# Optimization experiments

Hardware: AMD Instinct MI355X
Metric: run time of the kernel (lower is better)

The kernel has to match this reference:

```python
import jax, jax.numpy as jnp
import numpy as np

N_NODES = 50000
N_EDGES = 800000
N_IN = 256
N_H = 64


def _xavier(key, fan_in, fan_out):
    limit = np.sqrt(6.0 / (fan_in + fan_out)).astype(np.float32)
    return jax.random.uniform(key, (fan_in, fan_out), jnp.float32, -limit, limit)


def setup_inputs() -> dict:
    key = jax.random.key(0)
    ks = jax.random.split(key, 12)
    inp = {
        "bf": jax.random.normal(ks[0], (1, N_NODES, N_IN), jnp.float32),
        "bl": jax.random.normal(ks[1], (1, N_NODES, N_IN), jnp.float32),
        "shuf_fts": jax.random.normal(ks[2], (1, N_NODES, N_IN), jnp.float32),
        "shuf_fls": jax.random.normal(ks[3], (1, N_NODES, N_IN), jnp.float32),
        "adj_rows": jax.random.randint(ks[4], (N_EDGES,), 0, N_NODES, jnp.int32),
        "adj_cols": jax.random.randint(ks[5], (N_EDGES,), 0, N_NODES, jnp.int32),
        "adj_w": jax.random.uniform(ks[6], (N_EDGES,), jnp.float32),
        "diff_rows": jax.random.randint(ks[7], (N_EDGES,), 0, N_NODES, jnp.int32),
        "diff_cols": jax.random.randint(ks[8], (N_EDGES,), 0, N_NODES, jnp.int32),
        "diff_w": jax.random.uniform(ks[9], (N_EDGES,), jnp.float32),
        # GCN parameters (Linear has bias=False; separate additive bias init 0; PReLU slope 0.25)
        "W1": _xavier(ks[10], N_IN, N_H),
        "b1": jnp.zeros((N_H,), jnp.float32),
        "a1": jnp.float32(0.25),
        "W2": _xavier(ks[11], N_IN, N_H),
        "b2": jnp.zeros((N_H,), jnp.float32),
        "a2": jnp.float32(0.25),
    }
    return inp


def _gcn(seq, W, b, a, rows, cols, w):
    # seq: [1, N, F_in]; sparse spmm: out[r] = sum_e 1[rows[e]==r] * w[e] * fts[cols[e]]
    fts = seq[0] @ W                                   # [N, n_h]
    msgs = w[:, None] * fts[cols]                      # [E, n_h] gather
    agg = jax.ops.segment_sum(msgs, rows, num_segments=N_NODES)  # [N, n_h] scatter-add
    out = agg[None, :, :] + b                          # bias add
    return jnp.where(out >= 0, out, a * out)           # PReLU


def reference(bf, bl, shuf_fts, shuf_fls, adj_rows, adj_cols, adj_w,
              diff_rows, diff_cols, diff_w, W1, b1, a1, W2, b2, a2):
    h_1 = _gcn(bf, W1, b1, a1, adj_rows, adj_cols, adj_w)
    h_2 = _gcn(bl, W2, b2, a2, diff_rows, diff_cols, diff_w)
    h_3 = _gcn(shuf_fts, W1, b1, a1, adj_rows, adj_cols, adj_w)
    h_4 = _gcn(shuf_fls, W2, b2, a2, diff_rows, diff_cols, diff_w)
    return jnp.stack([h_1, h_2, h_3, h_4])             # [4, 1, N, n_h]
```

## Files before the change

kernel.cpp:

```cpp
#include <hip/hip_runtime.h>
#include <hip/hip_bf16.h>

#define N_NODES 50000
#define N_EDGES 800000
#define N_IN    256
#define N_H     64
#define NB      125
#define RPB     400
#define BCAP    8192
#define EPT     8
#define BIN_BLK 2048
#define GSTRIDE 264

typedef short short8 __attribute__((ext_vector_type(8)));
typedef float f32x4  __attribute__((ext_vector_type(4)));

__device__ inline short f2bf(float f) {
    __bf16 h = (__bf16)f;
    return (short)__builtin_bit_cast(unsigned short, h);
}
__device__ inline float bflo(unsigned int q) { return __uint_as_float(q << 16); }
__device__ inline float bfhi(unsigned int q) { return __uint_as_float(q & 0xFFFF0000u); }


__global__ __launch_bounds__(256) void k_bin(
    const int* __restrict__ adj_rows, const int* __restrict__ adj_cols,
    const float* __restrict__ adj_w,
    const int* __restrict__ diff_rows, const int* __restrict__ diff_cols,
    const float* __restrict__ diff_w,
    int* __restrict__ gcnt, int2* __restrict__ bin) {

    int g = blockIdx.y;
    const int*   rows = g ? diff_rows : adj_rows;
    const int*   cols = g ? diff_cols : adj_cols;
    const float* ww   = g ? diff_w    : adj_w;
    int base_e = blockIdx.x * BIN_BLK;
    int t = threadIdx.x;

    __shared__ int lcnt[NB];
    __shared__ int lbase[NB];
    for (int i = t; i < NB; i += 256) lcnt[i] = 0;
    __syncthreads();

    int lpos[EPT];
    int bkt[EPT];
    #pragma unroll
    for (int e = 0; e < EPT; ++e) {
        int idx = base_e + e * 256 + t;
        if (idx < N_EDGES) {
            int r = rows[idx];
            int b = r / RPB;
            bkt[e] = b;
            lpos[e] = atomicAdd(&lcnt[b], 1);
        } else bkt[e] = -1;
    }
    __syncthreads();
    for (int i = t; i < NB; i += 256) lbase[i] = atomicAdd(&gcnt[g * NB + i], lcnt[i]);
    __syncthreads();

    #pragma unroll
    for (int e = 0; e < EPT; ++e) {
        int idx = base_e + e * 256 + t;
        if (idx < N_EDGES) {
            unsigned int r = (unsigned int)rows[idx];
            unsigned int c = (unsigned int)cols[idx];
            int b = bkt[e];
            int2 m;
            m.x = (int)((r << 16) | c);
            m.y = __float_as_int(ww[idx]);
            bin[((size_t)(g * NB + b)) * BCAP + lbase[b] + lpos[e]] = m;
        }
    }
}


__global__ __launch_bounds__(256) void k_build(
    const int* __restrict__ gcnt, const int2* __restrict__ bin,
    int2* __restrict__ csr, int* __restrict__ row_ptr) {

    int g = blockIdx.y, b = blockIdx.x, t = threadIdx.x;
    __shared__ int hist[512];
    __shared__ int s2[256];
    __shared__ int sbase;

    for (int i = t; i < 512; i += 256) hist[i] = 0;
    __syncthreads();

    int cnt = gcnt[g * NB + b];
    const int2* be = bin + ((size_t)(g * NB + b)) * BCAP;
    int r0 = b * RPB;

    for (int i = t; i < cnt; i += 256) {
        unsigned int rc = (unsigned int)be[i].x;
        atomicAdd(&hist[(rc >> 16) - r0], 1);
    }
    __syncthreads();

    if (t == 0) {
        int s = 0;
        for (int i = 0; i < b; ++i) s += gcnt[g * NB + i];
        sbase = s;
    }

    int v0 = hist[2 * t], v1 = hist[2 * t + 1];
    int local = v0 + v1;
    s2[t] = local;
    __syncthreads();
    for (int off = 1; off < 256; off <<= 1) {
        int v = (t >= off) ? s2[t - off] : 0;
        __syncthreads();
        s2[t] += v;
        __syncthreads();
    }
    int e0 = sbase + (s2[t] - local);
    int e1 = e0 + v0;

    int* rp = row_ptr + g * (N_NODES + 1);
    if (2 * t < RPB)     rp[r0 + 2 * t]     = e0;
    if (2 * t + 1 < RPB) rp[r0 + 2 * t + 1] = e1;
    __syncthreads();
    hist[2 * t] = e0;
    hist[2 * t + 1] = e1;
    __syncthreads();

    int2* cg = csr + (size_t)g * N_EDGES;
    for (int i = t; i < cnt; i += 256) {
        int2 m = be[i];
        unsigned int rc = (unsigned int)m.x;
        int lr = (int)(rc >> 16) - r0;
        int pos = atomicAdd(&hist[lr], 1);
        int2 o;
        o.x = (int)(rc & 0xFFFFu);
        o.y = m.y;
        cg[pos] = o;
    }
    if (b == NB - 1 && t == 0) rp[N_NODES] = N_EDGES;
}


__global__ __launch_bounds__(256) void k_wt(const float* __restrict__ W1,
                                            const float* __restrict__ W2,
                                            unsigned short* __restrict__ WTg) {
    int g = blockIdx.x;
    const float* W = g ? W2 : W1;
    unsigned short* o = WTg + (size_t)g * 64 * GSTRIDE;
    for (int i = threadIdx.x; i < N_IN * N_H; i += 256) {
        int k = i >> 6, c = i & 63;
        o[c * GSTRIDE + k] = (unsigned short)f2bf(W[i]);
    }
}


__global__ __launch_bounds__(512, 6) void k_gemm(
    const float* __restrict__ X0, const float* __restrict__ X1,
    const float* __restrict__ X2, const float* __restrict__ X3,
    const unsigned short* __restrict__ WTg,
    unsigned short* __restrict__ Tadj, unsigned short* __restrict__ Tdiff) {

    int g = blockIdx.y;
    const float* Xa = g ? X1 : X0;
    const float* Xb = g ? X3 : X2;
    unsigned short* T = g ? Tdiff : Tadj;
    const unsigned short* src = WTg + (size_t)g * 64 * GSTRIDE;

    __shared__ __align__(16) unsigned short WT[64 * GSTRIDE];
    {
        const uint4* s4 = (const uint4*)src;
        uint4* d4 = (uint4*)WT;
        int t = threadIdx.x;
        #pragma unroll
        for (int j = 0; j < 4; ++j) d4[t + 512 * j] = s4[t + 512 * j];
        if (t < 64) d4[2048 + t] = s4[2048 + t];
    }
    __syncthreads();

    int wid  = threadIdx.x >> 6;
    int lane = threadIdx.x & 63;
    int rb = blockIdx.x * 128 + wid * 16;
    if (rb >= N_NODES) return;

    int arow = rb + (lane & 15);
    int kg   = lane >> 4;
    const float* apa = Xa + (size_t)arow * N_IN + kg * 8;
    const float* apb = Xb + (size_t)arow * N_IN + kg * 8;

    f32x4 acc[2][4];
    #pragma unroll
    for (int s = 0; s < 2; ++s)
        #pragma unroll
        for (int ct = 0; ct < 4; ++ct) acc[s][ct] = (f32x4){0.f, 0.f, 0.f, 0.f};

    for (int kt = 0; kt < 8; ++kt) {
        const float4* pa = reinterpret_cast<const float4*>(apa + kt * 32);
        const float4* pb = reinterpret_cast<const float4*>(apb + kt * 32);
        float4 a0 = pa[0];
        float4 a1 = pa[1];
        float4 c0 = pb[0];
        float4 c1 = pb[1];
        short8 afa, afb;
        afa[0] = f2bf(a0.x); afa[1] = f2bf(a0.y); afa[2] = f2bf(a0.z); afa[3] = f2bf(a0.w);
        afa[4] = f2bf(a1.x); afa[5] = f2bf(a1.y); afa[6] = f2bf(a1.z); afa[7] = f2bf(a1.w);
        afb[0] = f2bf(c0.x); afb[1] = f2bf(c0.y); afb[2] = f2bf(c0.z); afb[3] = f2bf(c0.w);
        afb[4] = f2bf(c1.x); afb[5] = f2bf(c1.y); afb[6] = f2bf(c1.z); afb[7] = f2bf(c1.w);
        #pragma unroll
        for (int ct = 0; ct < 4; ++ct) {
            const unsigned short* wp = &WT[(ct * 16 + (lane & 15)) * GSTRIDE + kt * 32 + kg * 8];
            short8 bfr = *reinterpret_cast<const short8*>(wp);
            acc[0][ct] = __builtin_amdgcn_mfma_f32_16x16x32_bf16(afa, bfr, acc[0][ct], 0, 0, 0);
            acc[1][ct] = __builtin_amdgcn_mfma_f32_16x16x32_bf16(afb, bfr, acc[1][ct], 0, 0, 0);
        }
    }

    int rgrp = lane >> 4;
    #pragma unroll
    for (int ct = 0; ct < 4; ++ct) {
        int col = ct * 16 + (lane & 15);
        #pragma unroll
        for (int r = 0; r < 4; ++r) {
            int row = rb + rgrp * 4 + r;
            if (row < N_NODES) {
                T[(size_t)row * 128 + col]      = (unsigned short)f2bf(acc[0][ct][r]);
                T[(size_t)row * 128 + 64 + col] = (unsigned short)f2bf(acc[1][ct][r]);
            }
        }
    }
}


__global__ __launch_bounds__(256) void k_agg(
    const int* __restrict__ row_ptr, const int2* __restrict__ csr,
    const unsigned int* __restrict__ Tadj, const unsigned int* __restrict__ Tdiff,
    const float* __restrict__ b1, const float* __restrict__ a1,
    const float* __restrict__ b2, const float* __restrict__ a2,
    float* __restrict__ out) {

    int wid  = threadIdx.x >> 6;
    int lane = threadIdx.x & 63;
    int node = blockIdx.x * 4 + wid;
    int g    = blockIdx.y;

    const int* rp = row_ptr + g * (N_NODES + 1);
    const int2* el = csr + (size_t)g * N_EDGES;
    const unsigned int* Tu = g ? Tdiff : Tadj;

    int e  = rp[node];
    int e1 = rp[node + 1];
    float ax = 0.f, ay = 0.f;

    for (; e + 4 <= e1; e += 4) {
        int2 m0 = el[e + 0], m1 = el[e + 1], m2 = el[e + 2], m3 = el[e + 3];
        unsigned int q0 = Tu[(size_t)m0.x * 64 + lane];
        unsigned int q1 = Tu[(size_t)m1.x * 64 + lane];
        unsigned int q2 = Tu[(size_t)m2.x * 64 + lane];
        unsigned int q3 = Tu[(size_t)m3.x * 64 + lane];
        float w0 = __int_as_float(m0.y), w1 = __int_as_float(m1.y);
        float w2 = __int_as_float(m2.y), w3 = __int_as_float(m3.y);
        ax += w0 * bflo(q0); ay += w0 * bfhi(q0);
        ax += w1 * bflo(q1); ay += w1 * bfhi(q1);
        ax += w2 * bflo(q2); ay += w2 * bfhi(q2);
        ax += w3 * bflo(q3); ay += w3 * bfhi(q3);
    }
    for (; e < e1; ++e) {
        int2 m = el[e];
        unsigned int q = Tu[(size_t)m.x * 64 + lane];
        float w = __int_as_float(m.y);
        ax += w * bflo(q); ay += w * bfhi(q);
    }

    const float* bias = g ? b2 : b1;
    float slope = g ? a2[0] : a1[0];
    int f = 2 * lane;
    size_t base;
    int fo;
    if (lane < 32) { base = g ? (size_t)3200000 : (size_t)0;       fo = f; }
    else           { base = g ? (size_t)9600000 : (size_t)6400000; fo = f - 64; }
    float v0 = ax + bias[fo];
    float v1 = ay + bias[fo + 1];
    v0 = (v0 >= 0.f) ? v0 : slope * v0;
    v1 = (v1 >= 0.f) ? v1 : slope * v1;
    float2 res; res.x = v0; res.y = v1;
    *reinterpret_cast<float2*>(out + base + (size_t)node * 64 + fo) = res;
}


extern "C" void kernel_launch(void* const* d_in, const int* in_sizes, int n_in,
                              void* d_out, int out_size, void* d_ws, size_t ws_size,
                              hipStream_t stream) {
    const float* bf_      = (const float*)d_in[0];
    const float* bl_      = (const float*)d_in[1];
    const float* shuf_fts = (const float*)d_in[2];
    const float* shuf_fls = (const float*)d_in[3];
    const int*   adj_rows = (const int*)d_in[4];
    const int*   adj_cols = (const int*)d_in[5];
    const float* adj_w    = (const float*)d_in[6];
    const int*   diff_rows= (const int*)d_in[7];
    const int*   diff_cols= (const int*)d_in[8];
    const float* diff_w   = (const float*)d_in[9];
    const float* W1       = (const float*)d_in[10];
    const float* b1       = (const float*)d_in[11];
    const float* a1       = (const float*)d_in[12];
    const float* W2       = (const float*)d_in[13];
    const float* b2       = (const float*)d_in[14];
    const float* a2       = (const float*)d_in[15];
    float* out = (float*)d_out;

    char* ws = (char*)d_ws;
    unsigned short* Tadj  = (unsigned short*)(ws);
    unsigned short* Tdiff = (unsigned short*)(ws + 12800000);
    int2* csr             = (int2*)(ws + 25600000);
    int*  row_ptr         = (int*)(ws + 38400000);
    int*  gcnt            = (int*)(ws + 38801024);
    unsigned short* WTg   = (unsigned short*)(ws + 38803072);

    int2* bin = (int2*)d_out;

    hipMemsetAsync(gcnt, 0, 2 * NB * sizeof(int), stream);

    k_bin<<<dim3((N_EDGES + BIN_BLK - 1) / BIN_BLK, 2), dim3(256), 0, stream>>>(
        adj_rows, adj_cols, adj_w, diff_rows, diff_cols, diff_w, gcnt, bin);
    k_wt<<<dim3(2), dim3(256), 0, stream>>>(W1, W2, WTg);
    k_build<<<dim3(NB, 2), dim3(256), 0, stream>>>(gcnt, bin, csr, row_ptr);

    k_gemm<<<dim3((N_NODES + 127) / 128, 2), dim3(512), 0, stream>>>(
        bf_, bl_, shuf_fts, shuf_fls, WTg, Tadj, Tdiff);

    k_agg<<<dim3(N_NODES / 4, 2), dim3(256), 0, stream>>>(
        row_ptr, csr, (const unsigned int*)Tadj, (const unsigned int*)Tdiff,
        b1, a1, b2, a2, out);
}
```

Before: 216.7 us.

## Split GEMM waves per input and preload whole A row into registers

Each wave now handles one of the two input matrices for 16 rows rather than both, doubling the number of blocks. All 16 float4 loads of the A row are issued up front into registers before the MFMA loop, so the loads are in flight together instead of being spread across the k-loop. The launch-bounds occupancy hint drops from 6 to 4 to leave room for the larger register footprint. Each block now loads the shared W tile for half as many rows, which doubles that LDS-fill overhead.

```diff
diff --git a/kernel.cpp b/kernel.cpp
--- a/kernel.cpp
+++ b/kernel.cpp
@@ -151,15 +151,13 @@
 }
 
 
-__global__ __launch_bounds__(512, 6) void k_gemm(
+__global__ __launch_bounds__(512, 4) void k_gemm(
     const float* __restrict__ X0, const float* __restrict__ X1,
     const float* __restrict__ X2, const float* __restrict__ X3,
     const unsigned short* __restrict__ WTg,
     unsigned short* __restrict__ Tadj, unsigned short* __restrict__ Tdiff) {
 
     int g = blockIdx.y;
-    const float* Xa = g ? X1 : X0;
-    const float* Xb = g ? X3 : X2;
     unsigned short* T = g ? Tdiff : Tadj;
     const unsigned short* src = WTg + (size_t)g * 64 * GSTRIDE;
 
@@ -169,59 +167,61 @@
         uint4* d4 = (uint4*)WT;
         int t = threadIdx.x;
         #pragma unroll
-        for (int j = 0; j < 4; ++j) d4[t + 512 * j] = s4[t + 512 * j];
+        for (int j = 0; j < 3; ++j) d4[t + 512 * j] = s4[t + 512 * j];
+        d4[t + 1536] = s4[t + 1536];
         if (t < 64) d4[2048 + t] = s4[2048 + t];
     }
     __syncthreads();
 
     int wid  = threadIdx.x >> 6;
     int lane = threadIdx.x & 63;
-    int rb = blockIdx.x * 128 + wid * 16;
+    int s    = wid & 1;
+    int rb   = blockIdx.x * 64 + (wid >> 1) * 16;
     if (rb >= N_NODES) return;
 
+    const float* X = s ? (g ? X3 : X2) : (g ? X1 : X0);
+    int coloff = s * 64;
+
     int arow = rb + (lane & 15);
+    if (arow >= N_NODES) arow = N_NODES - 1;
     int kg   = lane >> 4;
-    const float* apa = Xa + (size_t)arow * N_IN + kg * 8;
-    const float* apb = Xb + (size_t)arow * N_IN + kg * 8;
-
-    f32x4 acc[2][4];
-    #pragma unroll
-    for (int s = 0; s < 2; ++s)
-        #pragma unroll
-        for (int ct = 0; ct < 4; ++ct) acc[s][ct] = (f32x4){0.f, 0.f, 0.f, 0.f};
-
+    const float4* p = reinterpret_cast<const float4*>(X + (size_t)arow * N_IN) + kg * 2;
+
+    float4 rx[16];
+    #pragma unroll
     for (int kt = 0; kt < 8; ++kt) {
-        const float4* pa = reinterpret_cast<const float4*>(apa + kt * 32);
-        const float4* pb = reinterpret_cast<const float4*>(apb + kt * 32);
-        float4 a0 = pa[0];
-        float4 a1 = pa[1];
-        float4 c0 = pb[0];
-        float4 c1 = pb[1];
-        short8 afa, afb;
-        afa[0] = f2bf(a0.x); afa[1] = f2bf(a0.y); afa[2] = f2bf(a0.z); afa[3] = f2bf(a0.w);
-        afa[4] = f2bf(a1.x); afa[5] = f2bf(a1.y); afa[6] = f2bf(a1.z); afa[7] = f2bf(a1.w);
-        afb[0] = f2bf(c0.x); afb[1] = f2bf(c0.y); afb[2] = f2bf(c0.z); afb[3] = f2bf(c0.w);
-        afb[4] = f2bf(c1.x); afb[5] = f2bf(c1.y); afb[6] = f2bf(c1.z); afb[7] = f2bf(c1.w);
+        rx[2 * kt]     = p[kt * 8];
+        rx[2 * kt + 1] = p[kt * 8 + 1];
+    }
+
+    f32x4 acc[4];
+    #pragma unroll
+    for (int ct = 0; ct < 4; ++ct) acc[ct] = (f32x4){0.f, 0.f, 0.f, 0.f};
+
+    #pragma unroll
+    for (int kt = 0; kt < 8; ++kt) {
+        float4 a0 = rx[2 * kt];
+        float4 a1 = rx[2 * kt + 1];
+        short8 af;
+        af[0] = f2bf(a0.x); af[1] = f2bf(a0.y); af[2] = f2bf(a0.z); af[3] = f2bf(a0.w);
+        af[4] = f2bf(a1.x); af[5] = f2bf(a1.y); af[6] = f2bf(a1.z); af[7] = f2bf(a1.w);
         #pragma unroll
         for (int ct = 0; ct < 4; ++ct) {
             const unsigned short* wp = &WT[(ct * 16 + (lane & 15)) * GSTRIDE + kt * 32 + kg * 8];
             short8 bfr = *reinterpret_cast<const short8*>(wp);
-            acc[0][ct] = __builtin_amdgcn_mfma_f32_16x16x32_bf16(afa, bfr, acc[0][ct], 0, 0, 0);
-            acc[1][ct] = __builtin_amdgcn_mfma_f32_16x16x32_bf16(afb, bfr, acc[1][ct], 0, 0, 0);
+            acc[ct] = __builtin_amdgcn_mfma_f32_16x16x32_bf16(af, bfr, acc[ct], 0, 0, 0);
         }
     }
 
     int rgrp = lane >> 4;
     #pragma unroll
     for (int ct = 0; ct < 4; ++ct) {
-        int col = ct * 16 + (lane & 15);
+        int col = coloff + ct * 16 + (lane & 15);
         #pragma unroll
         for (int r = 0; r < 4; ++r) {
             int row = rb + rgrp * 4 + r;
-            if (row < N_NODES) {
-                T[(size_t)row * 128 + col]      = (unsigned short)f2bf(acc[0][ct][r]);
-                T[(size_t)row * 128 + 64 + col] = (unsigned short)f2bf(acc[1][ct][r]);
-            }
+            if (row < N_NODES)
+                T[(size_t)row * 128 + col] = (unsigned short)f2bf(acc[ct][r]);
         }
     }
 }
@@ -321,7 +321,7 @@
     k_wt<<<dim3(2), dim3(256), 0, stream>>>(W1, W2, WTg);
     k_build<<<dim3(NB, 2), dim3(256), 0, stream>>>(gcnt, bin, csr, row_ptr);
 
-    k_gemm<<<dim3((N_NODES + 127) / 128, 2), dim3(512), 0, stream>>>(
+    k_gemm<<<dim3((N_NODES + 63) / 64, 2), dim3(512), 0, stream>>>(
         bf_, bl_, shuf_fts, shuf_fls, WTg, Tadj, Tdiff);
 
     k_agg<<<dim3(N_NODES / 4, 2), dim3(256), 0, stream>>>(
```

Result: faster. 209.5 us (-3.3%).
